# Optimization experiments

Measured on AMD Instinct MI355X. Metric: run time of the kernel, lower is better.

The kernel has to match this reference:

```python
import jax, jax.numpy as jnp
import numpy as np

N_NODES = 100000
N_EDGES = 1600000
HIDDEN = 128
IN_CH = 128


def setup_inputs() -> dict:
    key = jax.random.key(0)
    ks = jax.random.split(key, 7)
    x = jax.random.normal(ks[0], (N_NODES, IN_CH), dtype=jnp.float32)
    # edge_index with no self-loops (col != row), matching remove_self_loops
    row = jax.random.randint(ks[1], (N_EDGES,), 0, N_NODES)
    off = jax.random.randint(ks[2], (N_EDGES,), 1, N_NODES)
    col = (row + off) % N_NODES
    edge_index = jnp.stack([row, col], axis=0).astype(jnp.int64)
    Wi = jax.random.normal(ks[3], (HIDDEN, IN_CH), dtype=jnp.float32) * (1.0 / np.sqrt(IN_CH))
    bi = jax.random.normal(ks[4], (HIDDEN,), dtype=jnp.float32) * 0.01
    A = jax.random.normal(ks[5], (HIDDEN, HIDDEN), dtype=jnp.float32) * (1.0 / np.sqrt(HIDDEN))
    Wp = jax.random.normal(ks[6], (HIDDEN, HIDDEN + 2), dtype=jnp.float32) * (1.0 / np.sqrt(HIDDEN))
    return {"x": x, "edge_index": edge_index, "Wi": Wi, "bi": bi, "A": A,
            "Wp": Wp, "num_layers": 4}


def _pairwise_weight(Wp):
    # W0: strictly-upper part symmetrized; diag = q * row-abs-sum + r
    W0 = jnp.triu(Wp[:, :-2], 1)
    W0 = W0 + W0.T
    q = Wp[:, -2]
    r = Wp[:, -1]
    return W0 + jnp.diag(q * jnp.sum(jnp.abs(W0), axis=1) + r)


def reference(x, edge_index, Wi, bi, A, Wp, num_layers):
    n = x.shape[0]
    row, col = edge_index[0], edge_index[1]
    # degree-based symmetric normalization (degree of target nodes)
    deg = jax.ops.segment_sum(jnp.ones_like(col, dtype=x.dtype), col, num_segments=n)
    dinv = jnp.where(deg > 0, jax.lax.rsqrt(jnp.maximum(deg, 1.0)), 0.0)
    norm = dinv[row] * dinv[col]  # [edges]

    Weff = _pairwise_weight(Wp)          # symmetric [H, H]
    Asym = A - A.T                       # antisymmetric [H, H]

    h = jax.nn.relu(x @ Wi.T + bi)       # input projection (dropout eval = id)
    for _ in range(num_layers):
        out = h @ Weff.T                 # symmetric aggr pre-mix
        msg = norm[:, None] * out[row]   # gather + per-edge scale [E, H]
        agg = jax.ops.segment_sum(msg, col, num_segments=n)  # scatter-add
        delta = agg - jax.nn.relu(h @ Asym.T)
        h = h + jax.nn.relu(jnp.tanh(delta))
    return h
```

## Files before the change

### kernel.cpp

```cpp
#include <hip/hip_runtime.h>
#include <hip/hip_bf16.h>

#define HID 128
#define NLAYERS 4
#define SCHUNK 2048

typedef __attribute__((ext_vector_type(8))) short bf16x8;
typedef __attribute__((ext_vector_type(4))) float f32x4;

__device__ __forceinline__ float bf2f(unsigned short u) {
    union { unsigned int i; float f; } v; v.i = ((unsigned int)u) << 16; return v.f;
}
__device__ __forceinline__ unsigned short f2bf(float f) {
    union { float f; unsigned int i; } v; v.f = f;
    unsigned int r = v.i + 0x7FFF + ((v.i >> 16) & 1);
    return (unsigned short)(r >> 16);
}

__global__ void k_detect(const unsigned int* ei, int* flag) {
    __shared__ int s;
    if (threadIdx.x == 0) s = 1;
    __syncthreads();
    unsigned int w = ei[threadIdx.x * 2 + 1];
    if (w != 0) s = 0;
    __syncthreads();
    if (threadIdx.x == 0) *flag = s;
}

__global__ void k_convert_edges(const void* ei, const int* flag, int* row32, int* col32,
                                int* deg, int ne) {
    int e = blockIdx.x * blockDim.x + threadIdx.x;
    if (e >= ne) return;
    int r, c;
    if (*flag) {
        const long long* p = (const long long*)ei;
        r = (int)p[e];
        c = (int)p[(size_t)ne + e];
    } else {
        const int* p = (const int*)ei;
        r = p[e];
        c = p[(size_t)ne + e];
    }
    row32[e] = r;
    col32[e] = c;
    atomicAdd(&deg[c], 1);
}

__global__ void k_scan1(const int* deg, int* partial, float* dinv, int n) {
    int tid = threadIdx.x, lane = tid & 63, wid = tid >> 6;
    int i0 = blockIdx.x * SCHUNK + tid * 8;
    int ts = 0;
    #pragma unroll
    for (int j = 0; j < 8; ++j) {
        int i = i0 + j;
        if (i < n) {
            int d = deg[i];
            ts += d;
            dinv[i] = (d > 0) ? rsqrtf((float)d) : 0.f;
        }
    }
    #pragma unroll
    for (int m = 1; m < 64; m <<= 1) ts += __shfl_xor(ts, m);
    __shared__ int ws[4];
    if (lane == 0) ws[wid] = ts;
    __syncthreads();
    if (tid == 0) partial[blockIdx.x] = ws[0] + ws[1] + ws[2] + ws[3];
}

__global__ void k_scan2(int* partial, int nb) {
    int tid = threadIdx.x;
    int v = (tid < nb) ? partial[tid] : 0;
    int s = v;
    #pragma unroll
    for (int off = 1; off < 64; off <<= 1) {
        int t = __shfl_up(s, off);
        if (tid >= off) s += t;
    }
    if (tid < nb) partial[tid] = s - v;
}

__global__ void k_scan3(const int* deg, const int* partial, int* offs, int* pos, int n, int ne) {
    int tid = threadIdx.x, lane = tid & 63, wid = tid >> 6;
    int i0 = blockIdx.x * SCHUNK + tid * 8;
    int v[8], ts = 0;
    #pragma unroll
    for (int j = 0; j < 8; ++j) { v[j] = (i0 + j < n) ? deg[i0 + j] : 0; ts += v[j]; }
    int s = ts;
    #pragma unroll
    for (int off = 1; off < 64; off <<= 1) { int t = __shfl_up(s, off); if (lane >= off) s += t; }
    __shared__ int ws[4];
    if (lane == 63) ws[wid] = s;
    __syncthreads();
    int run = partial[blockIdx.x] + (s - ts);
    for (int w = 0; w < wid; ++w) run += ws[w];
    #pragma unroll
    for (int j = 0; j < 8; ++j) {
        if (i0 + j < n) { offs[i0 + j] = run; pos[i0 + j] = run; }
        run += v[j];
    }
    if (blockIdx.x == 0 && tid == 0) offs[n] = ne;
}

__global__ void k_csrfill(const int* row32, const int* col32, int* pos, int* csr, int ne) {
    int e = blockIdx.x * blockDim.x + threadIdx.x;
    if (e >= ne) return;
    int c = col32[e];
    int p = atomicAdd(&pos[c], 1);
    csr[p] = row32[e];
}

__global__ void k_weff(const float* Wp, unsigned short* WeffB) {
    int i = threadIdx.x;
    const float* wr = Wp + i * 130;
    float rs = 0.f;
    for (int j = 0; j < 128; ++j) {
        float w = (i < j) ? wr[j] : ((i > j) ? Wp[j * 130 + i] : 0.f);
        rs += fabsf(w);
    }
    float q = wr[128], r = wr[129];
    for (int j = 0; j < 128; ++j) {
        float w = (i < j) ? wr[j] : ((i > j) ? Wp[j * 130 + i] : (q * rs + r));
        WeffB[i * 128 + j] = f2bf(w);
    }
}

__global__ void k_asym_wi(const float* A, const float* Wi, unsigned short* AsymB, unsigned short* WiB) {
    int idx = blockIdx.x * blockDim.x + threadIdx.x;
    if (idx >= 16384) return;
    int i = idx >> 7, j = idx & 127;
    AsymB[idx] = f2bf(A[idx] - A[j * 128 + i]);
    WiB[idx] = f2bf(Wi[idx]);
}

__global__ void k_convx(const float* x, unsigned short* xb, int n4) {
    int i = blockIdx.x * blockDim.x + threadIdx.x;
    if (i >= n4) return;
    float4 v = ((const float4*)x)[i];
    ushort4 o;
    o.x = f2bf(v.x); o.y = f2bf(v.y); o.z = f2bf(v.z); o.w = f2bf(v.w);
    ((ushort4*)xb)[i] = o;
}

__launch_bounds__(256, 2)
__global__ void k_gemm0(const unsigned short* xb, const unsigned short* WiB, const float* bi,
                        float* h, unsigned short* hb, int n) {
    int wid = threadIdx.x >> 6, lane = threadIdx.x & 63;
    int row0 = blockIdx.x * 64 + wid * 16;
    int lrow = lane & 15, lk = (lane >> 4) * 8;
    int arow = row0 + lrow; if (arow >= n) arow = n - 1;
    const bf16x8* Aptr = (const bf16x8*)(xb + (size_t)arow * 128);
    f32x4 acc[8];
    #pragma unroll
    for (int cf = 0; cf < 8; ++cf) acc[cf] = (f32x4)(0.f);
    #pragma unroll
    for (int kk = 0; kk < 4; ++kk) {
        bf16x8 a = Aptr[kk * 4 + (lk >> 3)];
        #pragma unroll
        for (int cf = 0; cf < 8; ++cf) {
            bf16x8 b = *(const bf16x8*)(WiB + (size_t)(cf * 16 + lrow) * 128 + kk * 32 + lk);
            acc[cf] = __builtin_amdgcn_mfma_f32_16x16x32_bf16(a, b, acc[cf], 0, 0, 0);
        }
    }
    int orow_base = row0 + (lane >> 4) * 4;
    #pragma unroll
    for (int r = 0; r < 4; ++r) {
        int orow = orow_base + r;
        if (orow >= n) continue;
        #pragma unroll
        for (int cf = 0; cf < 8; ++cf) {
            int col = cf * 16 + lrow;
            float v = acc[cf][r] + bi[col];
            v = fmaxf(v, 0.f);
            h[(size_t)orow * 128 + col] = v;
            hb[(size_t)orow * 128 + col] = f2bf(v);
        }
    }
}

__launch_bounds__(256, 2)
__global__ void k_gemm_dual(const unsigned short* hb, const unsigned short* WeffB,
                            const unsigned short* AsymB, const float* dinv,
                            unsigned short* outSs, unsigned short* zrelu, int n) {
    int wid = threadIdx.x >> 6, lane = threadIdx.x & 63;
    int row0 = blockIdx.x * 64 + wid * 16;
    int lrow = lane & 15, lk = (lane >> 4) * 8;
    int arow = row0 + lrow; if (arow >= n) arow = n - 1;
    const bf16x8* Aptr = (const bf16x8*)(hb + (size_t)arow * 128);
    f32x4 acc0[8], acc1[8];
    #pragma unroll
    for (int cf = 0; cf < 8; ++cf) { acc0[cf] = (f32x4)(0.f); acc1[cf] = (f32x4)(0.f); }
    #pragma unroll
    for (int kk = 0; kk < 4; ++kk) {
        bf16x8 a = Aptr[kk * 4 + (lk >> 3)];
        #pragma unroll
        for (int cf = 0; cf < 8; ++cf) {
            bf16x8 b0 = *(const bf16x8*)(WeffB + (size_t)(cf * 16 + lrow) * 128 + kk * 32 + lk);
            acc0[cf] = __builtin_amdgcn_mfma_f32_16x16x32_bf16(a, b0, acc0[cf], 0, 0, 0);
            bf16x8 b1 = *(const bf16x8*)(AsymB + (size_t)(cf * 16 + lrow) * 128 + kk * 32 + lk);
            acc1[cf] = __builtin_amdgcn_mfma_f32_16x16x32_bf16(a, b1, acc1[cf], 0, 0, 0);
        }
    }
    int orow_base = row0 + (lane >> 4) * 4;
    #pragma unroll
    for (int r = 0; r < 4; ++r) {
        int orow = orow_base + r;
        if (orow >= n) continue;
        float dv = dinv[orow];
        #pragma unroll
        for (int cf = 0; cf < 8; ++cf) {
            int col = cf * 16 + lrow;
            outSs[(size_t)orow * 128 + col] = f2bf(acc0[cf][r] * dv);
            zrelu[(size_t)orow * 128 + col] = f2bf(fmaxf(acc1[cf][r], 0.f));
        }
    }
}

__launch_bounds__(256, 8)
__global__ void k_aggregate(const unsigned short* outSs, const unsigned short* zrelu,
                            const int* csr, const int* offs, const float* dinv,
                            float* h, unsigned short* hb, int n) {
    int wid = threadIdx.x >> 6, lane = threadIdx.x & 63;
    int c = blockIdx.x * 4 + wid;
    if (c >= n) return;
    int g = lane >> 4;
    int fl = lane & 15;
    int s = offs[c], e = offs[c + 1];
    float accA[8], accB[8];
    #pragma unroll
    for (int k = 0; k < 8; ++k) { accA[k] = 0.f; accB[k] = 0.f; }
    int j = s;
    for (; j + 8 <= e; j += 8) {
        int r0 = csr[j + g];
        int r1 = csr[j + 4 + g];
        uint4 v0 = *(const uint4*)(outSs + (size_t)r0 * 128 + fl * 8);
        uint4 v1 = *(const uint4*)(outSs + (size_t)r1 * 128 + fl * 8);
        accA[0] += bf2f((unsigned short)(v0.x & 0xffff)); accA[1] += bf2f((unsigned short)(v0.x >> 16));
        accA[2] += bf2f((unsigned short)(v0.y & 0xffff)); accA[3] += bf2f((unsigned short)(v0.y >> 16));
        accA[4] += bf2f((unsigned short)(v0.z & 0xffff)); accA[5] += bf2f((unsigned short)(v0.z >> 16));
        accA[6] += bf2f((unsigned short)(v0.w & 0xffff)); accA[7] += bf2f((unsigned short)(v0.w >> 16));
        accB[0] += bf2f((unsigned short)(v1.x & 0xffff)); accB[1] += bf2f((unsigned short)(v1.x >> 16));
        accB[2] += bf2f((unsigned short)(v1.y & 0xffff)); accB[3] += bf2f((unsigned short)(v1.y >> 16));
        accB[4] += bf2f((unsigned short)(v1.z & 0xffff)); accB[5] += bf2f((unsigned short)(v1.z >> 16));
        accB[6] += bf2f((unsigned short)(v1.w & 0xffff)); accB[7] += bf2f((unsigned short)(v1.w >> 16));
    }
    for (; j < e; j += 4) {
        int idx = j + g;
        if (idx < e) {
            int r = csr[idx];
            uint4 v = *(const uint4*)(outSs + (size_t)r * 128 + fl * 8);
            accA[0] += bf2f((unsigned short)(v.x & 0xffff)); accA[1] += bf2f((unsigned short)(v.x >> 16));
            accA[2] += bf2f((unsigned short)(v.y & 0xffff)); accA[3] += bf2f((unsigned short)(v.y >> 16));
            accA[4] += bf2f((unsigned short)(v.z & 0xffff)); accA[5] += bf2f((unsigned short)(v.z >> 16));
            accA[6] += bf2f((unsigned short)(v.w & 0xffff)); accA[7] += bf2f((unsigned short)(v.w >> 16));
        }
    }
    #pragma unroll
    for (int k = 0; k < 8; ++k) {
        float a = accA[k] + accB[k];
        a += __shfl_xor(a, 16);
        a += __shfl_xor(a, 32);
        accA[k] = a;
    }
    int f0 = fl * 8 + g * 2;
    float dv = dinv[c];
    unsigned int z = *(const unsigned int*)(zrelu + (size_t)c * 128 + f0);
    float d0 = dv * accA[g * 2]     - bf2f((unsigned short)(z & 0xffff));
    float d1 = dv * accA[g * 2 + 1] - bf2f((unsigned short)(z >> 16));
    float u0 = fmaxf(tanhf(d0), 0.f);
    float u1 = fmaxf(tanhf(d1), 0.f);
    size_t base = (size_t)c * 128 + f0;
    float2 hv = *(const float2*)(h + base);
    hv.x += u0; hv.y += u1;
    *(float2*)(h + base) = hv;
    *(unsigned int*)(hb + base) = ((unsigned int)f2bf(hv.y) << 16) | (unsigned int)f2bf(hv.x);
}

extern "C" void kernel_launch(void* const* d_in, const int* in_sizes, int n_in,
                              void* d_out, int out_size, void* d_ws, size_t ws_size,
                              hipStream_t stream) {
    const float* x  = (const float*)d_in[0];
    const void*  ei = d_in[1];
    const float* Wi = (const float*)d_in[2];
    const float* bi = (const float*)d_in[3];
    const float* A  = (const float*)d_in[4];
    const float* Wp = (const float*)d_in[5];

    const int n  = in_sizes[0] / HID;
    const int ne = in_sizes[1] / 2;

    char* w = (char*)d_ws;
    size_t o = 0;
    auto alloc = [&](size_t bytes) -> void* {
        void* p = w + o;
        o = (o + bytes + 255) & ~(size_t)255;
        return p;
    };
    int*            flag    = (int*)alloc(4);
    int*            row32   = (int*)alloc((size_t)ne * 4);
    int*            col32   = (int*)alloc((size_t)ne * 4);
    int*            deg     = (int*)alloc((size_t)n * 4);
    float*          dinv    = (float*)alloc((size_t)n * 4);
    int*            offs    = (int*)alloc((size_t)(n + 1) * 4);
    int*            pos     = (int*)alloc((size_t)n * 4);
    int*            partial = (int*)alloc(64 * 4);
    int*            csr     = (int*)alloc((size_t)ne * 4);
    unsigned short* WeffB   = (unsigned short*)alloc(16384 * 2);
    unsigned short* AsymB   = (unsigned short*)alloc(16384 * 2);
    unsigned short* WiB     = (unsigned short*)alloc(16384 * 2);
    unsigned short* hb      = (unsigned short*)alloc((size_t)n * 128 * 2);
    unsigned short* outSs   = (unsigned short*)alloc((size_t)n * 128 * 2);
    unsigned short* zrelu   = (unsigned short*)alloc((size_t)n * 128 * 2);
    if (o > ws_size) return;

    float* h = (float*)d_out;

    hipMemsetAsync(deg, 0, (size_t)n * 4, stream);

    int eb = (ne + 255) / 256;
    int sb = (n + SCHUNK - 1) / SCHUNK;

    k_detect<<<1, 256, 0, stream>>>((const unsigned int*)ei, flag);
    k_convert_edges<<<eb, 256, 0, stream>>>(ei, flag, row32, col32, deg, ne);
    k_scan1<<<sb, 256, 0, stream>>>(deg, partial, dinv, n);
    k_scan2<<<1, 64, 0, stream>>>(partial, sb);
    k_scan3<<<sb, 256, 0, stream>>>(deg, partial, offs, pos, n, ne);
    k_csrfill<<<eb, 256, 0, stream>>>(row32, col32, pos, csr, ne);
    k_weff<<<1, 128, 0, stream>>>(Wp, WeffB);
    k_asym_wi<<<64, 256, 0, stream>>>(A, Wi, AsymB, WiB);

    int n4 = n * 128 / 4;
    k_convx<<<(n4 + 255) / 256, 256, 0, stream>>>(x, hb, n4);

    int gb = (n + 63) / 64;
    k_gemm0<<<gb, 256, 0, stream>>>(hb, WiB, bi, h, hb, n);

    int ab = (n + 3) / 4;
    for (int l = 0; l < NLAYERS; ++l) {
        k_gemm_dual<<<gb, 256, 0, stream>>>(hb, WeffB, AsymB, dinv, outSs, zrelu, n);
        k_aggregate<<<ab, 256, 0, stream>>>(outSs, zrelu, csr, offs, dinv, h, hb, n);
    }
}
```

Measured before the change: 871.3 us.

## Window CSR fill atomics by destination range and deepen aggregate gather unroll

```diff
diff --git a/kernel.cpp b/kernel.cpp
--- a/kernel.cpp
+++ b/kernel.cpp
@@ -4,6 +4,7 @@
 #define HID 128
 #define NLAYERS 4
 #define SCHUNK 2048
+#define WSHIFT 13
 
 typedef __attribute__((ext_vector_type(8))) short bf16x8;
 typedef __attribute__((ext_vector_type(4))) float f32x4;
@@ -101,12 +102,25 @@
     if (blockIdx.x == 0 && tid == 0) offs[n] = ne;
 }
 
-__global__ void k_csrfill(const int* row32, const int* col32, int* pos, int* csr, int ne) {
-    int e = blockIdx.x * blockDim.x + threadIdx.x;
-    if (e >= ne) return;
-    int c = col32[e];
-    int p = atomicAdd(&pos[c], 1);
-    csr[p] = row32[e];
+__global__ void k_csrfill(const int* row32, const int* col32, int* pos, int* csr,
+                          int ne, int nwin) {
+    int e0 = (blockIdx.x * blockDim.x + threadIdx.x) * 4;
+    int r[4], c[4], w[4];
+    #pragma unroll
+    for (int k = 0; k < 4; ++k) {
+        int e = e0 + k;
+        if (e < ne) { c[k] = col32[e]; r[k] = row32[e]; w[k] = c[k] >> WSHIFT; }
+        else w[k] = -1;
+    }
+    for (int p = 0; p < nwin; ++p) {
+        #pragma unroll
+        for (int k = 0; k < 4; ++k) {
+            if (w[k] == p) {
+                int q = atomicAdd(&pos[c[k]], 1);
+                csr[q] = r[k];
+            }
+        }
+    }
 }
 
 __global__ void k_weff(const float* Wp, unsigned short* WeffB) {
@@ -229,11 +243,15 @@
     #pragma unroll
     for (int k = 0; k < 8; ++k) { accA[k] = 0.f; accB[k] = 0.f; }
     int j = s;
-    for (; j + 8 <= e; j += 8) {
+    for (; j + 16 <= e; j += 16) {
         int r0 = csr[j + g];
         int r1 = csr[j + 4 + g];
+        int r2 = csr[j + 8 + g];
+        int r3 = csr[j + 12 + g];
         uint4 v0 = *(const uint4*)(outSs + (size_t)r0 * 128 + fl * 8);
         uint4 v1 = *(const uint4*)(outSs + (size_t)r1 * 128 + fl * 8);
+        uint4 v2 = *(const uint4*)(outSs + (size_t)r2 * 128 + fl * 8);
+        uint4 v3 = *(const uint4*)(outSs + (size_t)r3 * 128 + fl * 8);
         accA[0] += bf2f((unsigned short)(v0.x & 0xffff)); accA[1] += bf2f((unsigned short)(v0.x >> 16));
         accA[2] += bf2f((unsigned short)(v0.y & 0xffff)); accA[3] += bf2f((unsigned short)(v0.y >> 16));
         accA[4] += bf2f((unsigned short)(v0.z & 0xffff)); accA[5] += bf2f((unsigned short)(v0.z >> 16));
@@ -242,16 +260,32 @@
         accB[2] += bf2f((unsigned short)(v1.y & 0xffff)); accB[3] += bf2f((unsigned short)(v1.y >> 16));
         accB[4] += bf2f((unsigned short)(v1.z & 0xffff)); accB[5] += bf2f((unsigned short)(v1.z >> 16));
         accB[6] += bf2f((unsigned short)(v1.w & 0xffff)); accB[7] += bf2f((unsigned short)(v1.w >> 16));
-    }
-    for (; j < e; j += 4) {
-        int idx = j + g;
-        if (idx < e) {
-            int r = csr[idx];
+        accA[0] += bf2f((unsigned short)(v2.x & 0xffff)); accA[1] += bf2f((unsigned short)(v2.x >> 16));
+        accA[2] += bf2f((unsigned short)(v2.y & 0xffff)); accA[3] += bf2f((unsigned short)(v2.y >> 16));
+        accA[4] += bf2f((unsigned short)(v2.z & 0xffff)); accA[5] += bf2f((unsigned short)(v2.z >> 16));
+        accA[6] += bf2f((unsigned short)(v2.w & 0xffff)); accA[7] += bf2f((unsigned short)(v2.w >> 16));
+        accB[0] += bf2f((unsigned short)(v3.x & 0xffff)); accB[1] += bf2f((unsigned short)(v3.x >> 16));
+        accB[2] += bf2f((unsigned short)(v3.y & 0xffff)); accB[3] += bf2f((unsigned short)(v3.y >> 16));
+        accB[4] += bf2f((unsigned short)(v3.z & 0xffff)); accB[5] += bf2f((unsigned short)(v3.z >> 16));
+        accB[6] += bf2f((unsigned short)(v3.w & 0xffff)); accB[7] += bf2f((unsigned short)(v3.w >> 16));
+    }
+    for (; j < e; j += 8) {
+        int i0 = j + g, i1 = j + 4 + g;
+        if (i0 < e) {
+            int r = csr[i0];
             uint4 v = *(const uint4*)(outSs + (size_t)r * 128 + fl * 8);
             accA[0] += bf2f((unsigned short)(v.x & 0xffff)); accA[1] += bf2f((unsigned short)(v.x >> 16));
             accA[2] += bf2f((unsigned short)(v.y & 0xffff)); accA[3] += bf2f((unsigned short)(v.y >> 16));
             accA[4] += bf2f((unsigned short)(v.z & 0xffff)); accA[5] += bf2f((unsigned short)(v.z >> 16));
             accA[6] += bf2f((unsigned short)(v.w & 0xffff)); accA[7] += bf2f((unsigned short)(v.w >> 16));
+        }
+        if (i1 < e) {
+            int r = csr[i1];
+            uint4 v = *(const uint4*)(outSs + (size_t)r * 128 + fl * 8);
+            accB[0] += bf2f((unsigned short)(v.x & 0xffff)); accB[1] += bf2f((unsigned short)(v.x >> 16));
+            accB[2] += bf2f((unsigned short)(v.y & 0xffff)); accB[3] += bf2f((unsigned short)(v.y >> 16));
+            accB[4] += bf2f((unsigned short)(v.z & 0xffff)); accB[5] += bf2f((unsigned short)(v.z >> 16));
+            accB[6] += bf2f((unsigned short)(v.w & 0xffff)); accB[7] += bf2f((unsigned short)(v.w >> 16));
         }
     }
     #pragma unroll
@@ -318,13 +352,15 @@
 
     int eb = (ne + 255) / 256;
     int sb = (n + SCHUNK - 1) / SCHUNK;
+    int nwin = (n + (1 << WSHIFT) - 1) >> WSHIFT;
 
     k_detect<<<1, 256, 0, stream>>>((const unsigned int*)ei, flag);
     k_convert_edges<<<eb, 256, 0, stream>>>(ei, flag, row32, col32, deg, ne);
     k_scan1<<<sb, 256, 0, stream>>>(deg, partial, dinv, n);
     k_scan2<<<1, 64, 0, stream>>>(partial, sb);
     k_scan3<<<sb, 256, 0, stream>>>(deg, partial, offs, pos, n, ne);
-    k_csrfill<<<eb, 256, 0, stream>>>(row32, col32, pos, csr, ne);
+    int fb = (ne + 1023) / 1024;
+    k_csrfill<<<fb, 256, 0, stream>>>(row32, col32, pos, csr, ne, nwin);
     k_weff<<<1, 128, 0, stream>>>(Wp, WeffB);
     k_asym_wi<<<64, 256, 0, stream>>>(A, Wi, AsymB, WiB);
 
```

New measurement: 840.2 us. 1.04x faster.
